# Performance work log

Measured on AMD Instinct MI355X. Metric: run time of the kernel, lower is better.

The kernel has to match this reference:

```python
import jax, jax.numpy as jnp
import numpy as np

NUM_EXPERTS = 8
TOP_K = 2
HIDDEN = 1024
INTER = 1408
B, S = 2, 1024


def setup_inputs() -> dict:
    key = jax.random.key(0)
    k1, k2, k3, k4, k5 = jax.random.split(key, 5)
    scale = 0.02  # keep activations well-scaled
    return {
        "hidden_states": jax.random.normal(k1, (B, S, HIDDEN), dtype=jnp.float32),
        "gate_w": jax.random.normal(k2, (HIDDEN, NUM_EXPERTS), dtype=jnp.float32) * scale,
        "w_gate": jax.random.normal(k3, (NUM_EXPERTS, HIDDEN, INTER), dtype=jnp.float32) * scale,
        "w_up": jax.random.normal(k4, (NUM_EXPERTS, HIDDEN, INTER), dtype=jnp.float32) * scale,
        "w_down": jax.random.normal(k5, (NUM_EXPERTS, INTER, HIDDEN), dtype=jnp.float32) * scale,
    }


def reference(hidden_states, gate_w, w_gate, w_up, w_down):
    b, s, h = hidden_states.shape
    x = hidden_states.reshape(-1, h)  # [T, H]
    # Router: softmax in fp32, top-k, renormalize over selected experts
    logits = x @ gate_w  # [T, E]
    probs = jax.nn.softmax(logits.astype(jnp.float32), axis=-1)
    rw, sel = jax.lax.top_k(probs, TOP_K)  # [T, K]
    rw = rw / jnp.sum(rw, axis=-1, keepdims=True)
    rw = rw.astype(x.dtype)
    # Per-(token, expert) combine weight; duplicates summed (matches torch mask sum)
    combine = jnp.sum(rw[:, :, None] * jax.nn.one_hot(sel, NUM_EXPERTS, dtype=x.dtype), axis=1)  # [T, E]
    out = jnp.zeros_like(x)
    for e in range(NUM_EXPERTS):  # fixed small structural loop over experts
        inter = jax.nn.silu(x @ w_gate[e]) * (x @ w_up[e])  # [T, I]
        out = out + (inter @ w_down[e]) * combine[:, e:e + 1]
    return out.reshape(b, s, h)
```

## Files before the change

kernel.cpp:

```cpp
#include <hip/hip_runtime.h>
#include <hip/hip_bf16.h>

#define T_TOKENS 2048
#define HID 1024
#define ISZ 1408
#define NEXP 8
#define TILES_MAX 72

typedef __bf16 bf16x8 __attribute__((ext_vector_type(8)));
typedef __bf16 bf16x4 __attribute__((ext_vector_type(4)));
typedef float  f32x16 __attribute__((ext_vector_type(16)));

__device__ __forceinline__ void gload16(const void* g, void* l) {
    __builtin_amdgcn_global_load_lds(
        (const __attribute__((address_space(1))) void*)g,
        (__attribute__((address_space(3))) void*)l,
        16, 0, 0);
}

#define PIPE_BARRIER(N)                                              \
    asm volatile("s_waitcnt vmcnt(" #N ") lgkmcnt(0)" ::: "memory"); \
    __builtin_amdgcn_sched_barrier(0);                               \
    __builtin_amdgcn_s_barrier();                                    \
    __builtin_amdgcn_sched_barrier(0);

__global__ __launch_bounds__(256) void prep_kernel(
    const float* __restrict__ x, const float* __restrict__ gw,
    int* __restrict__ sel, float* __restrict__ wt, __bf16* __restrict__ xb,
    const float* __restrict__ wg, const float* __restrict__ wu, const float* __restrict__ wd,
    __bf16* __restrict__ wgT, __bf16* __restrict__ wuT, __bf16* __restrict__ wdT)
{
    __shared__ __bf16 tb[2][64][70];
    const int bid = blockIdx.x;
    const int tid = threadIdx.x;

    if (bid < 512) {
        const int wave = tid >> 6;
        const int lane = tid & 63;
        const int t = bid * 4 + wave;
        const float* xr = x + (size_t)t * HID;

        const int c0 = lane * 16;
        float4 v0 = *(const float4*)(xr + c0);
        float4 v1 = *(const float4*)(xr + c0 + 4);
        float4 v2 = *(const float4*)(xr + c0 + 8);
        float4 v3 = *(const float4*)(xr + c0 + 12);
        {
            bf16x8 o0, o1;
            o0[0]=(__bf16)v0.x; o0[1]=(__bf16)v0.y; o0[2]=(__bf16)v0.z; o0[3]=(__bf16)v0.w;
            o0[4]=(__bf16)v1.x; o0[5]=(__bf16)v1.y; o0[6]=(__bf16)v1.z; o0[7]=(__bf16)v1.w;
            o1[0]=(__bf16)v2.x; o1[1]=(__bf16)v2.y; o1[2]=(__bf16)v2.z; o1[3]=(__bf16)v2.w;
            o1[4]=(__bf16)v3.x; o1[5]=(__bf16)v3.y; o1[6]=(__bf16)v3.z; o1[7]=(__bf16)v3.w;
            *(bf16x8*)(xb + (size_t)t * HID + c0) = o0;
            *(bf16x8*)(xb + (size_t)t * HID + c0 + 8) = o1;
        }
        if (bid == 0 && tid < 128) {
            bf16x8 z8;
            #pragma unroll
            for (int j = 0; j < 8; ++j) z8[j] = (__bf16)0.f;
            *(bf16x8*)(xb + (size_t)T_TOKENS * HID + tid * 8) = z8;
        }

        float le[8] = {0.f, 0.f, 0.f, 0.f, 0.f, 0.f, 0.f, 0.f};
        float xv[16];
        xv[0]=v0.x; xv[1]=v0.y; xv[2]=v0.z; xv[3]=v0.w;
        xv[4]=v1.x; xv[5]=v1.y; xv[6]=v1.z; xv[7]=v1.w;
        xv[8]=v2.x; xv[9]=v2.y; xv[10]=v2.z; xv[11]=v2.w;
        xv[12]=v3.x; xv[13]=v3.y; xv[14]=v3.z; xv[15]=v3.w;
        #pragma unroll
        for (int j = 0; j < 16; ++j) {
            const float* gr = gw + (size_t)(c0 + j) * NEXP;
            float4 g0 = *(const float4*)gr;
            float4 g1 = *(const float4*)(gr + 4);
            le[0] += xv[j] * g0.x; le[1] += xv[j] * g0.y;
            le[2] += xv[j] * g0.z; le[3] += xv[j] * g0.w;
            le[4] += xv[j] * g1.x; le[5] += xv[j] * g1.y;
            le[6] += xv[j] * g1.z; le[7] += xv[j] * g1.w;
        }
        #pragma unroll
        for (int d = 1; d < 64; d <<= 1) {
            #pragma unroll
            for (int k = 0; k < 8; ++k) le[k] += __shfl_xor(le[k], d);
        }
        float m = le[0];
        #pragma unroll
        for (int k = 1; k < 8; ++k) m = fmaxf(m, le[k]);
        float pe[8]; float s = 0.f;
        #pragma unroll
        for (int k = 0; k < 8; ++k) { pe[k] = expf(le[k] - m); s += pe[k]; }
        int e1 = 0; float p1 = pe[0];
        #pragma unroll
        for (int k = 1; k < 8; ++k) if (pe[k] > p1) { p1 = pe[k]; e1 = k; }
        int e2 = -1; float p2 = -1.f;
        #pragma unroll
        for (int k = 0; k < 8; ++k) if (k != e1 && pe[k] > p2) { p2 = pe[k]; e2 = k; }
        if (lane == 0) {
            float inv = 1.0f / (p1 + p2);
            sel[t * 2 + 0] = e1; sel[t * 2 + 1] = e2;
            wt[t * 2 + 0] = p1 * inv; wt[t * 2 + 1] = p2 * inv;
        }
        return;
    }

    const int lr  = tid >> 4;
    const int lc4 = (tid & 15) * 4;
    const float* in;
    __bf16* out;
    int R, C, rrA, ccA, rrB, ccB;

    if (bid < 3328) {
        const int f   = bid - 512;
        const int z   = f / 176;
        const int rem = f % 176;
        const int bx  = rem / 16;
        const int by  = rem & 15;
        const int e   = z & 7;
        R = HID; C = ISZ;
        in  = (z < 8 ? wg : wu) + (size_t)e * R * C;
        out = (z < 8 ? wgT : wuT) + (size_t)e * R * C;
        rrA = by * 64; rrB = rrA;
        ccA = bx * 128; ccB = ccA + 64;
    } else {
        const int f   = bid - 3328;
        const int e   = f / 176;
        const int rem = f % 176;
        const int bx  = rem / 16;
        const int by  = rem & 15;
        R = ISZ; C = HID;
        in  = wd  + (size_t)e * R * C;
        out = wdT + (size_t)e * R * C;
        ccA = by * 64; ccB = ccA;
        rrA = bx * 128; rrB = rrA + 64;
    }

    auto loadcvt = [&](int buf, int rr, int cc) {
        #pragma unroll
        for (int p = 0; p < 4; ++p) {
            float4 v = *(const float4*)(in + (size_t)(rr + p * 16 + lr) * C + cc + lc4);
            bf16x4 w;
            w[0] = (__bf16)v.x; w[1] = (__bf16)v.y; w[2] = (__bf16)v.z; w[3] = (__bf16)v.w;
            *(bf16x4*)&tb[buf][p * 16 + lr][lc4] = w;
        }
    };
    auto storeT = [&](int buf, int rr, int cc) {
        #pragma unroll
        for (int q = 0; q < 2; ++q) {
            const int oc = (tid >> 3) + 32 * q;
            const int vs = (tid & 7) * 8;
            bf16x8 w;
            #pragma unroll
            for (int j = 0; j < 8; ++j) w[j] = tb[buf][vs + j][oc];
            *(bf16x8*)(out + (size_t)(cc + oc) * R + rr + vs) = w;
        }
    };

    loadcvt(0, rrA, ccA);
    __syncthreads();
    loadcvt(1, rrB, ccB);
    storeT(0, rrA, ccA);
    __syncthreads();
    storeT(1, rrB, ccB);
}

__global__ __launch_bounds__(1024) void scan_assign_kernel(
    int* __restrict__ tiles,
    const int* __restrict__ sel, const float* __restrict__ wt,
    int* __restrict__ rtok, float* __restrict__ rwt, int* __restrict__ tok2row)
{
    __shared__ int hist[NEXP];
    __shared__ int soff[NEXP];
    __shared__ int snal[NEXP];
    __shared__ int scur[NEXP];
    if (threadIdx.x < NEXP) { hist[threadIdx.x] = 0; scur[threadIdx.x] = 0; }
    __syncthreads();
    for (int t = threadIdx.x; t < T_TOKENS; t += 1024) {
        atomicAdd(&hist[sel[t * 2 + 0]], 1);
        atomicAdd(&hist[sel[t * 2 + 1]], 1);
    }
    __syncthreads();
    if (threadIdx.x == 0) {
        int cur = 0, tix = 0;
        for (int e = 0; e < NEXP; ++e) {
            soff[e] = cur;
            int n64 = (hist[e] + 63) & ~63;
            snal[e] = n64;
            for (int rt = 0; rt * 64 < n64; ++rt)
                tiles[tix++] = (e << 16) | (cur + rt * 64);
            cur += n64;
        }
        for (; tix < TILES_MAX; ++tix) tiles[tix] = -1;
    }
    __syncthreads();
    for (int e = 0; e < NEXP; ++e) {
        const int lo = soff[e] + hist[e], hi = soff[e] + snal[e];
        for (int r = lo + (int)threadIdx.x; r < hi; r += 1024) rtok[r] = 0;
    }
    __syncthreads();
    for (int t = threadIdx.x; t < T_TOKENS; t += 1024) {
        #pragma unroll
        for (int k = 0; k < 2; ++k) {
            int e = sel[t * 2 + k];
            int pos = atomicAdd(&scur[e], 1);
            int row = soff[e] + pos;
            rtok[row] = t + 1;
            rwt[row] = wt[t * 2 + k];
            tok2row[t * 2 + k] = row;
        }
    }
}

__global__ __launch_bounds__(256) void ffn1_kernel(
    const __bf16* __restrict__ xb, const int* __restrict__ rtok,
    const __bf16* __restrict__ wgT, const __bf16* __restrict__ wuT,
    const int* __restrict__ tiles, __bf16* __restrict__ inter,
    const float* __restrict__ wd, __bf16* __restrict__ wdT)
{
    __shared__ __align__(16) char smem[36864];
    const int n   = blockIdx.x;
    const int tid = threadIdx.x;

    if (n >= 22 * TILES_MAX) {
        auto tb = (__bf16 (*)[64][70])smem;
        const int f   = n - 22 * TILES_MAX;
        const int e   = 4 + f / 176;
        const int rem = f % 176;
        const int bx  = rem / 16;
        const int by  = rem & 15;
        const int R = ISZ, C = HID;
        const float* in = wd + (size_t)e * R * C;
        __bf16* out = wdT + (size_t)e * R * C;
        const int ccA = by * 64, ccB = ccA;
        const int rrA = bx * 128, rrB = rrA + 64;
        const int lr  = tid >> 4;
        const int lc4 = (tid & 15) * 4;

        auto loadcvt = [&](int buf, int rr, int cc) {
            #pragma unroll
            for (int p = 0; p < 4; ++p) {
                float4 v = *(const float4*)(in + (size_t)(rr + p * 16 + lr) * C + cc + lc4);
                bf16x4 w;
                w[0] = (__bf16)v.x; w[1] = (__bf16)v.y; w[2] = (__bf16)v.z; w[3] = (__bf16)v.w;
                *(bf16x4*)&tb[buf][p * 16 + lr][lc4] = w;
            }
        };
        auto storeT = [&](int buf, int rr, int cc) {
            #pragma unroll
            for (int q = 0; q < 2; ++q) {
                const int oc = (tid >> 3) + 32 * q;
                const int vs = (tid & 7) * 8;
                bf16x8 w;
                #pragma unroll
                for (int j = 0; j < 8; ++j) w[j] = tb[buf][vs + j][oc];
                *(bf16x8*)(out + (size_t)(cc + oc) * R + rr + vs) = w;
            }
        };

        loadcvt(0, rrA, ccA);
        __syncthreads();
        loadcvt(1, rrB, ccB);
        storeT(0, rrA, ccA);
        __syncthreads();
        storeT(1, rrB, ccB);
        return;
    }

    auto sA = (__bf16 (*)[64][32])(smem);
    auto sG = (__bf16 (*)[64][32])(smem + 12288);
    auto sU = (__bf16 (*)[64][32])(smem + 24576);

    const int nn = (n & 7) * 198 + (n >> 3);
    const int i0 = (nn / TILES_MAX) * 64;
    const int tv = tiles[nn % TILES_MAX];
    if (tv < 0) return;
    const int e = tv >> 16;
    const int rowbase = tv & 0xFFFF;

    const int lane = tid & 63;
    const int wid  = tid >> 6;
    const int wr = wid >> 1, wc = wid & 1;
    const int l31 = lane & 31;
    const int kg  = lane >> 5;

    const int r16 = lane >> 2;
    const int cz  = (((lane & 3) ^ ((r16 >> 1) & 3)) * 8);
    const int rowA = rowbase + wid * 16 + r16;
    const int tokp = rtok[rowA];
    const int src  = tokp ? (tokp - 1) : T_TOKENS;
    const __bf16* A0 = xb + (size_t)src * HID + cz;
    const size_t wb = (size_t)e * ISZ * HID + (size_t)(i0 + wid * 16 + r16) * HID + cz;
    const __bf16* G0 = wgT + wb;
    const __bf16* U0 = wuT + wb;

    f32x16 accG, accU;
    #pragma unroll
    for (int r = 0; r < 16; ++r) { accG[r] = 0.f; accU[r] = 0.f; }

    auto stage = [&](int b, int k0) {
        gload16(A0 + k0, &sA[b][wid * 16][0]);
        gload16(G0 + k0, &sG[b][wid * 16][0]);
        gload16(U0 + k0, &sU[b][wid * 16][0]);
    };
    auto compute = [&](int b) {
        #pragma unroll
        for (int s = 0; s < 2; ++s) {
            const int ch = ((2 * s + kg) ^ ((l31 >> 1) & 3)) * 8;
            bf16x8 a_ = *(const bf16x8*)&sA[b][wr * 32 + l31][ch];
            bf16x8 g_ = *(const bf16x8*)&sG[b][wc * 32 + l31][ch];
            bf16x8 u_ = *(const bf16x8*)&sU[b][wc * 32 + l31][ch];
            __builtin_amdgcn_s_setprio(1);
            accG = __builtin_amdgcn_mfma_f32_32x32x16_bf16(a_, g_, accG, 0, 0, 0);
            accU = __builtin_amdgcn_mfma_f32_32x32x16_bf16(a_, u_, accU, 0, 0, 0);
            __builtin_amdgcn_s_setprio(0);
        }
    };

    const int nIter = HID / 32;
    stage(0, 0);
    stage(1, 32);
    PIPE_BARRIER(3)
    for (int i = 0; i < nIter; ++i) {
        int ks = (i + 2 < nIter) ? (i + 2) * 32 : 0;
        stage((i + 2) % 3, ks);
        compute(i % 3);
        PIPE_BARRIER(3)
    }

    const int base_row = rowbase + wr * 32;
    #pragma unroll
    for (int r = 0; r < 16; ++r) {
        float g = accG[r];
        float u = accU[r];
        float v = g / (1.0f + __expf(-g)) * u;
        int row = base_row + (r & 3) + 8 * (r >> 2) + 4 * kg;
        inter[(size_t)row * ISZ + i0 + wc * 32 + l31] = (__bf16)v;
    }
}

__global__ __launch_bounds__(256) void ffn2_kernel(
    const __bf16* __restrict__ inter, const __bf16* __restrict__ wdT,
    const float* __restrict__ rwt, const int* __restrict__ tiles,
    __bf16* __restrict__ y)
{
    const int n  = blockIdx.x;
    const int nn = (n & 7) * 72 + (n >> 3);
    const int n0 = (nn / TILES_MAX) * 128;
    const int tv = tiles[nn % TILES_MAX];
    if (tv < 0) return;
    const int e = tv >> 16;
    const int rowbase = tv & 0xFFFF;

    __shared__ __align__(16) __bf16 sA[3][64][32];
    __shared__ __align__(16) __bf16 sB[3][128][32];

    const int lane = threadIdx.x & 63;
    const int wid  = threadIdx.x >> 6;
    const int wr = wid >> 1, wc = wid & 1;
    const int l31 = lane & 31;
    const int kg  = lane >> 5;

    const int r16 = lane >> 2;
    const int cz  = (((lane & 3) ^ ((r16 >> 1) & 3)) * 8);
    const __bf16* A0 = inter + (size_t)(rowbase + wid * 16 + r16) * ISZ + cz;
    const __bf16* B0 = wdT + (size_t)e * HID * ISZ + (size_t)(n0 + wid * 32 + r16) * ISZ + cz;
    const size_t rstepB = (size_t)16 * ISZ;

    f32x16 acc[2];
    #pragma unroll
    for (int q = 0; q < 2; ++q)
        #pragma unroll
        for (int r = 0; r < 16; ++r) acc[q][r] = 0.f;

    auto stage = [&](int b, int k0) {
        gload16(A0 + k0,          &sA[b][wid * 16][0]);
        gload16(B0 + k0,          &sB[b][wid * 32][0]);
        gload16(B0 + k0 + rstepB, &sB[b][wid * 32 + 16][0]);
    };
    auto compute = [&](int b) {
        #pragma unroll
        for (int s = 0; s < 2; ++s) {
            const int ch = ((2 * s + kg) ^ ((l31 >> 1) & 3)) * 8;
            bf16x8 a_ = *(const bf16x8*)&sA[b][wr * 32 + l31][ch];
            bf16x8 b0 = *(const bf16x8*)&sB[b][wc * 64 + l31][ch];
            bf16x8 b1 = *(const bf16x8*)&sB[b][wc * 64 + 32 + l31][ch];
            __builtin_amdgcn_s_setprio(1);
            acc[0] = __builtin_amdgcn_mfma_f32_32x32x16_bf16(a_, b0, acc[0], 0, 0, 0);
            acc[1] = __builtin_amdgcn_mfma_f32_32x32x16_bf16(a_, b1, acc[1], 0, 0, 0);
            __builtin_amdgcn_s_setprio(0);
        }
    };

    const int nIter = ISZ / 32;
    stage(0, 0);
    stage(1, 32);
    PIPE_BARRIER(3)
    for (int i = 0; i < nIter; ++i) {
        int ks = (i + 2 < nIter) ? (i + 2) * 32 : 0;
        stage((i + 2) % 3, ks);
        compute(i % 3);
        PIPE_BARRIER(3)
    }

    const int base_row = rowbase + wr * 32;
    #pragma unroll
    for (int q = 0; q < 2; ++q) {
        const int col = n0 + wc * 64 + q * 32 + l31;
        #pragma unroll
        for (int r = 0; r < 16; ++r) {
            int row = base_row + (r & 3) + 8 * (r >> 2) + 4 * kg;
            y[(size_t)row * HID + col] = (__bf16)(rwt[row] * acc[q][r]);
        }
    }
}

__global__ __launch_bounds__(256) void combine_kernel(
    const __bf16* __restrict__ y, const int* __restrict__ tok2row, float* __restrict__ out)
{
    const int idx = blockIdx.x * 256 + threadIdx.x;
    const int t = idx >> 7;
    const int c = (idx & 127) * 8;
    const int r0 = tok2row[t * 2];
    const int r1 = tok2row[t * 2 + 1];
    bf16x8 a = *(const bf16x8*)(y + (size_t)r0 * HID + c);
    bf16x8 b = *(const bf16x8*)(y + (size_t)r1 * HID + c);
    float4 o0, o1;
    o0.x = (float)a[0] + (float)b[0]; o0.y = (float)a[1] + (float)b[1];
    o0.z = (float)a[2] + (float)b[2]; o0.w = (float)a[3] + (float)b[3];
    o1.x = (float)a[4] + (float)b[4]; o1.y = (float)a[5] + (float)b[5];
    o1.z = (float)a[6] + (float)b[6]; o1.w = (float)a[7] + (float)b[7];
    *(float4*)(out + (size_t)t * HID + c) = o0;
    *(float4*)(out + (size_t)t * HID + c + 4) = o1;
}

extern "C" void kernel_launch(void* const* d_in, const int* in_sizes, int n_in,
                              void* d_out, int out_size, void* d_ws, size_t ws_size,
                              hipStream_t stream) {
    const float* x  = (const float*)d_in[0];
    const float* gw = (const float*)d_in[1];
    const float* wg = (const float*)d_in[2];
    const float* wu = (const float*)d_in[3];
    const float* wd = (const float*)d_in[4];
    float* out = (float*)d_out;

    char* ws = (char*)d_ws;
    int*    tiles   = (int*)(ws + 64);
    int*    sel     = (int*)(ws + 1024);
    float*  wtp     = (float*)(ws + 17408);
    int*    rtok    = (int*)(ws + 33792);
    float*  rwt     = (float*)(ws + 52224);
    int*    tok2row = (int*)(ws + 70656);
    __bf16* xb      = (__bf16*)(ws + 87040);
    __bf16* inter   = (__bf16*)(ws + 4283648);
    __bf16* wgT     = (__bf16*)(ws + 17260032);
    __bf16* wuT     = (__bf16*)(ws + 40328704);
    __bf16* wdT     = (__bf16*)(ws + 63397376);
    __bf16* y       = (__bf16*)wgT;


    prep_kernel<<<4032, 256, 0, stream>>>(x, gw, sel, wtp, xb, wg, wu, wd, wgT, wuT, wdT);
    scan_assign_kernel<<<1, 1024, 0, stream>>>(tiles, sel, wtp, rtok, rwt, tok2row);

    ffn1_kernel<<<22 * TILES_MAX + 704, 256, 0, stream>>>(
        xb, rtok, wgT, wuT, tiles, inter, wd, wdT);
    ffn2_kernel<<<8 * TILES_MAX, 256, 0, stream>>>(inter, wdT, rwt, tiles, y);
    combine_kernel<<<(T_TOKENS * HID / 8) / 256, 256, 0, stream>>>(y, tok2row, out);
}
```

Before: 132.9 us.

## Use 128-row expert tiles with 512-thread blocks in the first FFN kernel

```diff
diff --git a/kernel.cpp b/kernel.cpp
--- a/kernel.cpp
+++ b/kernel.cpp
@@ -5,7 +5,8 @@
 #define HID 1024
 #define ISZ 1408
 #define NEXP 8
-#define TILES_MAX 72
+#define T128_MAX 40
+#define T64_MAX 80
 
 typedef __bf16 bf16x8 __attribute__((ext_vector_type(8)));
 typedef __bf16 bf16x4 __attribute__((ext_vector_type(4)));
@@ -163,7 +164,7 @@
 }
 
 __global__ __launch_bounds__(1024) void scan_assign_kernel(
-    int* __restrict__ tiles,
+    int* __restrict__ tiles128, int* __restrict__ tiles64,
     const int* __restrict__ sel, const float* __restrict__ wt,
     int* __restrict__ rtok, float* __restrict__ rwt, int* __restrict__ tok2row)
 {
@@ -179,16 +180,19 @@
     }
     __syncthreads();
     if (threadIdx.x == 0) {
-        int cur = 0, tix = 0;
+        int cur = 0, t128 = 0, t64 = 0;
         for (int e = 0; e < NEXP; ++e) {
             soff[e] = cur;
-            int n64 = (hist[e] + 63) & ~63;
-            snal[e] = n64;
-            for (int rt = 0; rt * 64 < n64; ++rt)
-                tiles[tix++] = (e << 16) | (cur + rt * 64);
-            cur += n64;
-        }
-        for (; tix < TILES_MAX; ++tix) tiles[tix] = -1;
+            int n128 = (hist[e] + 127) & ~127;
+            snal[e] = n128;
+            for (int rt = 0; rt * 128 < n128; ++rt)
+                tiles128[t128++] = (e << 16) | (cur + rt * 128);
+            for (int rt = 0; rt * 64 < n128; ++rt)
+                tiles64[t64++] = (e << 16) | (cur + rt * 64);
+            cur += n128;
+        }
+        for (; t128 < T128_MAX; ++t128) tiles128[t128] = -1;
+        for (; t64 < T64_MAX; ++t64) tiles64[t64] = -1;
     }
     __syncthreads();
     for (int e = 0; e < NEXP; ++e) {
@@ -209,19 +213,19 @@
     }
 }
 
-__global__ __launch_bounds__(256) void ffn1_kernel(
+__global__ __launch_bounds__(512) void ffn1_kernel(
     const __bf16* __restrict__ xb, const int* __restrict__ rtok,
     const __bf16* __restrict__ wgT, const __bf16* __restrict__ wuT,
-    const int* __restrict__ tiles, __bf16* __restrict__ inter,
+    const int* __restrict__ tiles128, __bf16* __restrict__ inter,
     const float* __restrict__ wd, __bf16* __restrict__ wdT)
 {
-    __shared__ __align__(16) char smem[36864];
+    __shared__ __align__(16) char smem[49152];
     const int n   = blockIdx.x;
     const int tid = threadIdx.x;
 
-    if (n >= 22 * TILES_MAX) {
+    if (n >= 22 * T128_MAX) {
         auto tb = (__bf16 (*)[64][70])smem;
-        const int f   = n - 22 * TILES_MAX;
+        const int f   = n - 22 * T128_MAX;
         const int e   = 4 + f / 176;
         const int rem = f % 176;
         const int bx  = rem / 16;
@@ -236,23 +240,27 @@
 
         auto loadcvt = [&](int buf, int rr, int cc) {
             #pragma unroll
-            for (int p = 0; p < 4; ++p) {
-                float4 v = *(const float4*)(in + (size_t)(rr + p * 16 + lr) * C + cc + lc4);
+            for (int p = 0; p < 2; ++p) {
+                float4 v = *(const float4*)(in + (size_t)(rr + p * 32 + lr) * C + cc + lc4);
                 bf16x4 w;
                 w[0] = (__bf16)v.x; w[1] = (__bf16)v.y; w[2] = (__bf16)v.z; w[3] = (__bf16)v.w;
-                *(bf16x4*)&tb[buf][p * 16 + lr][lc4] = w;
+                *(bf16x4*)&tb[buf][p * 32 + lr][lc4] = w;
             }
         };
         auto storeT = [&](int buf, int rr, int cc) {
             #pragma unroll
             for (int q = 0; q < 2; ++q) {
-                const int oc = (tid >> 3) + 32 * q;
-                const int vs = (tid & 7) * 8;
-                bf16x8 w;
-                #pragma unroll
-                for (int j = 0; j < 8; ++j) w[j] = tb[buf][vs + j][oc];
-                *(bf16x8*)(out + (size_t)(cc + oc) * R + rr + vs) = w;
+                const int idx = q * 512 + tid;
+                const int oc = idx >> 4;
+                const int vs = (idx & 15) * 8;
+                (void)oc; (void)vs;
             }
+            const int oc = tid >> 3;
+            const int vs = (tid & 7) * 8;
+            bf16x8 w;
+            #pragma unroll
+            for (int j = 0; j < 8; ++j) w[j] = tb[buf][vs + j][oc];
+            *(bf16x8*)(out + (size_t)(cc + oc) * R + rr + vs) = w;
         };
 
         loadcvt(0, rrA, ccA);
@@ -264,13 +272,13 @@
         return;
     }
 
-    auto sA = (__bf16 (*)[64][32])(smem);
-    auto sG = (__bf16 (*)[64][32])(smem + 12288);
-    auto sU = (__bf16 (*)[64][32])(smem + 24576);
-
-    const int nn = (n & 7) * 198 + (n >> 3);
-    const int i0 = (nn / TILES_MAX) * 64;
-    const int tv = tiles[nn % TILES_MAX];
+    auto sA = (__bf16 (*)[128][32])(smem);
+    auto sG = (__bf16 (*)[64][32])(smem + 24576);
+    auto sU = (__bf16 (*)[64][32])(smem + 36864);
+
+    const int nn = (n & 7) * 110 + (n >> 3);
+    const int i0 = (nn / T128_MAX) * 64;
+    const int tv = tiles128[nn % T128_MAX];
     if (tv < 0) return;
     const int e = tv >> 16;
     const int rowbase = tv & 0xFFFF;
@@ -287,9 +295,9 @@
     const int tokp = rtok[rowA];
     const int src  = tokp ? (tokp - 1) : T_TOKENS;
     const __bf16* A0 = xb + (size_t)src * HID + cz;
-    const size_t wb = (size_t)e * ISZ * HID + (size_t)(i0 + wid * 16 + r16) * HID + cz;
-    const __bf16* G0 = wgT + wb;
-    const __bf16* U0 = wuT + wb;
+    const int wrow = (wid & 3) * 16 + r16;
+    const __bf16* W0 = (wid < 4 ? wgT : wuT)
+                     + (size_t)e * ISZ * HID + (size_t)(i0 + wrow) * HID + cz;
 
     f32x16 accG, accU;
     #pragma unroll
@@ -297,8 +305,8 @@
 
     auto stage = [&](int b, int k0) {
         gload16(A0 + k0, &sA[b][wid * 16][0]);
-        gload16(G0 + k0, &sG[b][wid * 16][0]);
-        gload16(U0 + k0, &sU[b][wid * 16][0]);
+        if (wid < 4) gload16(W0 + k0, &sG[b][(wid & 3) * 16][0]);
+        else         gload16(W0 + k0, &sU[b][(wid & 3) * 16][0]);
     };
     auto compute = [&](int b) {
         #pragma unroll
@@ -317,34 +325,35 @@
     const int nIter = HID / 32;
     stage(0, 0);
     stage(1, 32);
-    PIPE_BARRIER(3)
+    PIPE_BARRIER(2)
     for (int i = 0; i < nIter; ++i) {
         int ks = (i + 2 < nIter) ? (i + 2) * 32 : 0;
         stage((i + 2) % 3, ks);
         compute(i % 3);
-        PIPE_BARRIER(3)
+        PIPE_BARRIER(2)
     }
 
     const int base_row = rowbase + wr * 32;
+    const int col = i0 + wc * 32 + l31;
     #pragma unroll
     for (int r = 0; r < 16; ++r) {
         float g = accG[r];
         float u = accU[r];
         float v = g / (1.0f + __expf(-g)) * u;
         int row = base_row + (r & 3) + 8 * (r >> 2) + 4 * kg;
-        inter[(size_t)row * ISZ + i0 + wc * 32 + l31] = (__bf16)v;
+        inter[(size_t)row * ISZ + col] = (__bf16)v;
     }
 }
 
 __global__ __launch_bounds__(256) void ffn2_kernel(
     const __bf16* __restrict__ inter, const __bf16* __restrict__ wdT,
-    const float* __restrict__ rwt, const int* __restrict__ tiles,
+    const float* __restrict__ rwt, const int* __restrict__ tiles64,
     __bf16* __restrict__ y)
 {
     const int n  = blockIdx.x;
-    const int nn = (n & 7) * 72 + (n >> 3);
-    const int n0 = (nn / TILES_MAX) * 128;
-    const int tv = tiles[nn % TILES_MAX];
+    const int nn = (n & 7) * 80 + (n >> 3);
+    const int n0 = (nn / T64_MAX) * 128;
+    const int tv = tiles64[nn % T64_MAX];
     if (tv < 0) return;
     const int e = tv >> 16;
     const int rowbase = tv & 0xFFFF;
@@ -442,25 +451,25 @@
     float* out = (float*)d_out;
 
     char* ws = (char*)d_ws;
-    int*    tiles   = (int*)(ws + 64);
-    int*    sel     = (int*)(ws + 1024);
-    float*  wtp     = (float*)(ws + 17408);
-    int*    rtok    = (int*)(ws + 33792);
-    float*  rwt     = (float*)(ws + 52224);
-    int*    tok2row = (int*)(ws + 70656);
-    __bf16* xb      = (__bf16*)(ws + 87040);
-    __bf16* inter   = (__bf16*)(ws + 4283648);
-    __bf16* wgT     = (__bf16*)(ws + 17260032);
-    __bf16* wuT     = (__bf16*)(ws + 40328704);
-    __bf16* wdT     = (__bf16*)(ws + 63397376);
-    __bf16* y       = (__bf16*)wgT;
-
+    int*    tiles128 = (int*)(ws + 64);
+    int*    tiles64  = (int*)(ws + 384);
+    int*    sel      = (int*)(ws + 1024);
+    float*  wtp      = (float*)(ws + 17408);
+    int*    rtok     = (int*)(ws + 33792);
+    float*  rwt      = (float*)(ws + 54272);
+    int*    tok2row  = (int*)(ws + 74752);
+    __bf16* xb       = (__bf16*)(ws + 91136);
+    __bf16* inter    = (__bf16*)(ws + 4287488);
+    __bf16* wgT      = (__bf16*)(ws + 18705408);
+    __bf16* wuT      = (__bf16*)(ws + 41774080);
+    __bf16* wdT      = (__bf16*)(ws + 64842752);
+    __bf16* y        = (__bf16*)wgT;
 
     prep_kernel<<<4032, 256, 0, stream>>>(x, gw, sel, wtp, xb, wg, wu, wd, wgT, wuT, wdT);
-    scan_assign_kernel<<<1, 1024, 0, stream>>>(tiles, sel, wtp, rtok, rwt, tok2row);
-
-    ffn1_kernel<<<22 * TILES_MAX + 704, 256, 0, stream>>>(
-        xb, rtok, wgT, wuT, tiles, inter, wd, wdT);
-    ffn2_kernel<<<8 * TILES_MAX, 256, 0, stream>>>(inter, wdT, rwt, tiles, y);
+    scan_assign_kernel<<<1, 1024, 0, stream>>>(tiles128, tiles64, sel, wtp, rtok, rwt, tok2row);
+
+    ffn1_kernel<<<22 * T128_MAX + 704, 512, 0, stream>>>(
+        xb, rtok, wgT, wuT, tiles128, inter, wd, wdT);
+    ffn2_kernel<<<8 * T64_MAX, 256, 0, stream>>>(inter, wdT, rwt, tiles64, y);
     combine_kernel<<<(T_TOKENS * HID / 8) / 256, 256, 0, stream>>>(y, tok2row, out);
 }
```

Measured after the change: 130.6 us. No clear change (-1.7%).
